# Kernel optimization log

Hardware: AMD Instinct MI355X
Metric: run time of the kernel (lower is better)

Reference implementation:

```python
import jax, jax.numpy as jnp
import numpy as np

R = 0.15          # ball-query radius (module init arg r)
K = 32            # _MAX_NEIGHBOURS
B, N = 8, 4096


def _ball_query(pos, r, k):
    """Dense ball query. pos: [B,N,3] -> neighbor idx [B,N,K], sorted by distance.
    Slots with fewer than k in-radius neighbors are filled with the query's own
    index (self is always the first neighbor at distance 0), so their
    contribution to (f_i - f_j)^2 is exactly 0 -- matching torch-points-kernels'
    fill-with-first-neighbor behaviour."""
    d2 = jnp.sum((pos[:, :, None, :] - pos[:, None, :, :]) ** 2, axis=-1)  # [B,N,N]
    masked = jnp.where(d2 <= r * r, d2, jnp.inf)
    neg_vals, idx = jax.lax.top_k(-masked, k)          # ascending distance
    valid = neg_vals > -jnp.inf
    self_idx = jnp.arange(pos.shape[1])[None, :, None]
    return jnp.where(valid, idx, self_idx)             # [B,N,K]


def setup_inputs() -> dict:
    key = jax.random.key(0)
    k1, k2 = jax.random.split(key)
    pos = jax.random.uniform(k1, (B, N, 3), dtype=jnp.float32)
    f = jax.random.normal(k2, (B, N), dtype=jnp.float32)
    return {"pos": pos, "f": f}


def reference(pos, f):
    # neighbor indices are non-differentiable (torch gathers with long indices)
    nei_idx = jax.lax.stop_gradient(_ball_query(pos, R, K))      # [B,N,K]
    f_nei = jax.vmap(lambda fb, ib: fb[ib])(f, nei_idx)          # [B,N,K]
    variances = jnp.sum((f[:, :, None] - f_nei) ** 2, axis=-1)   # [B,N]
    return 0.5 * jnp.mean(variances)
```

## Files before the change

### kernel.cpp

```cpp
#include <hip/hip_runtime.h>


#define BQ_K 32
#define CAP 128
#define WPB 8
#define G 6
#define NC (G * G * G)
#define CAPC 512
#define QMAX 64
#define NPTS 4096
#define NPART 64
#define PSTRIDE 16

__device__ __forceinline__ int cell_coord(float x) {
    int c = (int)(x * (float)G);
    return c < 0 ? 0 : (c > G - 1 ? G - 1 : c);
}

__device__ __forceinline__ unsigned int decode_cnt(unsigned int v) {
    return (v >= 0x80000000u) ? (v - 0xAAAAAAAAu) : v;
}

__device__ __forceinline__ float select_sum(float2 e0, float2 e1, int M,
                                            float r2) {
    if (M <= BQ_K) return e0.y + e1.y;
    float lo = 0.0f, hi = r2 * 1.000001f;
    #pragma unroll
    for (int it = 0; it < 12; ++it) {
        const float mid = 0.5f * (lo + hi);
        const int cnt = __popcll(__ballot(e0.x < mid)) +
                        __popcll(__ballot(e1.x < mid));
        if (cnt >= BQ_K) hi = mid; else lo = mid;
    }
    float s = 0.0f;
    if (e0.x < hi) s = e0.y;
    if (e1.x < hi) s += e1.y;
    return s;
}

__device__ __forceinline__ float dual_select_sum(
    float2 a0, float2 a1, int MA, float2 b0, float2 b1, int MB, float r2)
{
    const bool needA = MA > BQ_K;
    const bool needB = MB > BQ_K;
    float hiA = 1e31f, hiB = 1e31f;
    if (needA || needB) {
        float loA = 0.0f, loB = 0.0f;
        if (needA) hiA = r2 * 1.000001f;
        if (needB) hiB = r2 * 1.000001f;
        const bool bigA = MA > 64, bigB = MB > 64;
        #pragma unroll
        for (int it = 0; it < 12; ++it) {
            if (needA) {
                const float mid = 0.5f * (loA + hiA);
                int c = __popcll(__ballot(a0.x < mid));
                if (bigA) c += __popcll(__ballot(a1.x < mid));
                if (c >= BQ_K) hiA = mid; else loA = mid;
            }
            if (needB) {
                const float mid = 0.5f * (loB + hiB);
                int c = __popcll(__ballot(b0.x < mid));
                if (bigB) c += __popcll(__ballot(b1.x < mid));
                if (c >= BQ_K) hiB = mid; else loB = mid;
            }
        }
    }
    float s = 0.0f;
    if (a0.x < hiA) s += a0.y;
    if (a1.x < hiA) s += a1.y;
    if (b0.x < hiB) s += b0.y;
    if (b1.x < hiB) s += b1.y;
    return s;
}

__global__ __launch_bounds__(512, 8) void dl_fused8(
    const float* __restrict__ pos, const float* __restrict__ f,
    float* __restrict__ partial, unsigned int* __restrict__ c1,
    unsigned int* __restrict__ c2, float* __restrict__ out,
    float r2, float scale)
{
    __shared__ float4 s_cand[CAPC];
    __shared__ float2 s_sel[WPB][2][CAP];
    __shared__ int    s_q[QMAX];
    __shared__ int    s_ncand, s_nq;
    __shared__ float  s_wsum[WPB];
    __shared__ int    s_last;

    const int bc = blockIdx.x;
    const int b  = bc / NC;
    const int c  = bc - b * NC;
    const int cx = c % G, cy = (c / G) % G, cz = c / (G * G);

    const int lane = threadIdx.x & 63;
    const int wave = threadIdx.x >> 6;
    const unsigned long long lmask = (1ULL << lane) - 1ULL;

    if (threadIdx.x == 0) { s_ncand = 0; s_nq = 0; s_last = 0; }
    __syncthreads();

    const float* posb = pos + (size_t)b * NPTS * 3;
    const float* fb   = f   + (size_t)b * NPTS;

    const float lox = cx * (1.0f / G), hix = lox + (1.0f / G);
    const float loy = cy * (1.0f / G), hiy = loy + (1.0f / G);
    const float loz = cz * (1.0f / G), hiz = loz + (1.0f / G);

    constexpr int per = NPTS / WPB;
    const int wbeg = wave * per;
    for (int j0 = 0; j0 < per; j0 += 128) {
        const int ja = wbeg + j0 + lane;
        const int jb = ja + 64;
        const float xa = posb[3 * ja + 0];
        const float ya = posb[3 * ja + 1];
        const float za = posb[3 * ja + 2];
        const float fa = fb[ja];
        const float xb = posb[3 * jb + 0];
        const float yb = posb[3 * jb + 1];
        const float zb = posb[3 * jb + 2];
        const float fvb = fb[jb];

        const float dax = fmaxf(fmaxf(lox - xa, xa - hix), 0.0f);
        const float day = fmaxf(fmaxf(loy - ya, ya - hiy), 0.0f);
        const float daz = fmaxf(fmaxf(loz - za, za - hiz), 0.0f);
        const float d2a = fmaf(dax, dax, fmaf(day, day, daz * daz));
        const float dbx = fmaxf(fmaxf(lox - xb, xb - hix), 0.0f);
        const float dby = fmaxf(fmaxf(loy - yb, yb - hiy), 0.0f);
        const float dbz = fmaxf(fmaxf(loz - zb, zb - hiz), 0.0f);
        const float d2b = fmaf(dbx, dbx, fmaf(dby, dby, dbz * dbz));
        const bool ina = d2a <= r2;
        const bool inb = d2b <= r2;

        const unsigned long long ma = __ballot(ina);
        const unsigned long long mb = __ballot(inb);
        const int na = __popcll(ma);
        const int nh = na + __popcll(mb);
        int base = 0;
        if (lane == 0 && nh) base = atomicAdd(&s_ncand, nh);
        base = __shfl(base, 0, 64);
        if (ina) {
            const int off = base + __popcll(ma & lmask);
            if (off < CAPC) {
                s_cand[off] = make_float4(xa, ya, za, fa);
                if (cell_coord(xa) == cx && cell_coord(ya) == cy &&
                    cell_coord(za) == cz) {
                    const int qs = atomicAdd(&s_nq, 1);
                    if (qs < QMAX) s_q[qs] = off;
                }
            }
        }
        if (inb) {
            const int off = base + na + __popcll(mb & lmask);
            if (off < CAPC) {
                s_cand[off] = make_float4(xb, yb, zb, fvb);
                if (cell_coord(xb) == cx && cell_coord(yb) == cy &&
                    cell_coord(zb) == cz) {
                    const int qs = atomicAdd(&s_nq, 1);
                    if (qs < QMAX) s_q[qs] = off;
                }
            }
        }
    }
    __syncthreads();

    const int ncand = s_ncand < CAPC ? s_ncand : CAPC;
    const int nq    = s_nq < QMAX ? s_nq : QMAX;
    const int ncB   = (ncand + 63) & ~63;

    for (int i = ncand + threadIdx.x; i < ncB; i += 512)
        s_cand[i] = make_float4(1e30f, 1e30f, 1e30f, 0.0f);
    __syncthreads();

    float2* selA = s_sel[wave][0];
    float2* selB = s_sel[wave][1];
    float wsum = 0.0f;

    for (int qi = 2 * wave; qi < nq; qi += 2 * WPB) {
        const int  qj    = qi + 1;
        const bool haveB = qj < nq;
        const float4 qpA = s_cand[s_q[qi]];
        const float4 qpB = s_cand[s_q[haveB ? qj : qi]];
        const float qxA = qpA.x, qyA = qpA.y, qzA = qpA.z, fiA = qpA.w;
        const float qxB = qpB.x, qyB = qpB.y, qzB = qpB.z, fiB = qpB.w;

        int cinA = 0, cinB = 0;
        for (int basej = 0; basej < ncB; basej += 64) {
            const float4 cd = s_cand[basej + lane];
            const float dxA = cd.x - qxA, dyA = cd.y - qyA, dzA = cd.z - qzA;
            const float dxB = cd.x - qxB, dyB = cd.y - qyB, dzB = cd.z - qzB;
            const float d2A = fmaf(dxA, dxA, fmaf(dyA, dyA, dzA * dzA));
            const float d2B = fmaf(dxB, dxB, fmaf(dyB, dyB, dzB * dzB));
            const bool inbA = d2A <= r2;
            const bool inbB = haveB && (d2B <= r2);
            const unsigned long long mA = __ballot(inbA);
            const unsigned long long mB = __ballot(inbB);
            const int offA = cinA + __popcll(mA & lmask);
            const int offB = cinB + __popcll(mB & lmask);
            if (inbA && offA < CAP) {
                const float fd = fiA - cd.w;
                selA[offA] = make_float2(d2A, fd * fd);
            }
            if (inbB && offB < CAP) {
                const float fd = fiB - cd.w;
                selB[offB] = make_float2(d2B, fd * fd);
            }
            cinA += __popcll(mA);
            cinB += __popcll(mB);
        }
        const int MA = cinA < CAP ? cinA : CAP;
        const int MB = cinB < CAP ? cinB : CAP;
        const float2 a0 = (lane < MA) ? selA[lane] : make_float2(1e30f, 0.0f);
        const float2 a1 = (64 + lane < MA) ? selA[64 + lane]
                                           : make_float2(1e30f, 0.0f);
        const float2 b0 = (lane < MB) ? selB[lane] : make_float2(1e30f, 0.0f);
        const float2 b1 = (64 + lane < MB) ? selB[64 + lane]
                                           : make_float2(1e30f, 0.0f);
        wsum += dual_select_sum(a0, a1, MA, b0, b1, MB, r2);
    }

    for (int o = 32; o > 0; o >>= 1) wsum += __shfl_down(wsum, o, 64);
    if (lane == 0) s_wsum[wave] = wsum;
    __syncthreads();
    if (threadIdx.x == 0) {
        float bs = 0.0f;
        #pragma unroll
        for (int w = 0; w < WPB; ++w) bs += s_wsum[w];
        const int k = blockIdx.x & (NPART - 1);
        const float oldp = atomicAdd(&partial[k * PSTRIDE], bs);
        asm volatile("" :: "v"(oldp));
        const unsigned int expect = (gridDim.x - 1u - (unsigned)k) / 64u + 1u;
        const unsigned int oc =
            decode_cnt(atomicAdd(&c1[k * PSTRIDE], 1u));
        if (oc + 1u == expect) {
            const unsigned int o2 = decode_cnt(atomicAdd(c2, 1u));
            if (o2 + 1u == (unsigned)NPART)
                s_last = 1;
        }
    }
    __syncthreads();
    if (s_last && wave == 0) {
        float v = atomicAdd(&partial[lane * PSTRIDE], 0.0f);
        for (int o = 32; o > 0; o >>= 1) v += __shfl_down(v, o, 64);
        if (lane == 0) out[0] = v * scale;
    }
}

__global__ __launch_bounds__(256) void dl_fallback(
    const float* __restrict__ pos, const float* __restrict__ f,
    float* __restrict__ out, float r2, float scale)
{
    __shared__ float4 s_cand[CAPC];
    __shared__ float2 s_sel[4][CAP];
    __shared__ int    s_q[QMAX];
    __shared__ int    s_ncand, s_nq;
    __shared__ float  s_wsum[4];

    const int bc = blockIdx.x;
    const int b  = bc / NC;
    const int c  = bc - b * NC;
    const int cx = c % G, cy = (c / G) % G, cz = c / (G * G);
    const int lane = threadIdx.x & 63;
    const int wave = threadIdx.x >> 6;
    const unsigned long long lmask = (1ULL << lane) - 1ULL;

    if (threadIdx.x == 0) { s_ncand = 0; s_nq = 0; }
    __syncthreads();

    const float* posb = pos + (size_t)b * NPTS * 3;
    const float* fb   = f   + (size_t)b * NPTS;
    const float lox = cx * (1.0f / G), hix = lox + (1.0f / G);
    const float loy = cy * (1.0f / G), hiy = loy + (1.0f / G);
    const float loz = cz * (1.0f / G), hiz = loz + (1.0f / G);

    constexpr int per = NPTS / 4;
    const int wbeg = wave * per;
    for (int j0 = 0; j0 < per; j0 += 64) {
        const int j = wbeg + j0 + lane;
        const float x  = posb[3 * j + 0];
        const float y  = posb[3 * j + 1];
        const float z  = posb[3 * j + 2];
        const float ddx = fmaxf(fmaxf(lox - x, x - hix), 0.0f);
        const float ddy = fmaxf(fmaxf(loy - y, y - hiy), 0.0f);
        const float ddz = fmaxf(fmaxf(loz - z, z - hiz), 0.0f);
        const float d2c = fmaf(ddx, ddx, fmaf(ddy, ddy, ddz * ddz));
        const bool in = (d2c <= r2);
        const unsigned long long m = __ballot(in);
        const int nh = __popcll(m);
        int base = 0;
        if (lane == 0 && nh) base = atomicAdd(&s_ncand, nh);
        base = __shfl(base, 0, 64);
        if (in) {
            const int off = base + __popcll(m & lmask);
            if (off < CAPC) {
                s_cand[off] = make_float4(x, y, z, fb[j]);
                if (cell_coord(x) == cx && cell_coord(y) == cy &&
                    cell_coord(z) == cz) {
                    const int qs = atomicAdd(&s_nq, 1);
                    if (qs < QMAX) s_q[qs] = off;
                }
            }
        }
    }
    __syncthreads();

    const int ncand = s_ncand < CAPC ? s_ncand : CAPC;
    const int nq    = s_nq < QMAX ? s_nq : QMAX;
    const int ncB   = (ncand + 63) & ~63;
    float2* sel = s_sel[wave];
    float wsum = 0.0f;

    for (int qi = wave; qi < nq; qi += 4) {
        const float4 qp = s_cand[s_q[qi]];
        const float qx = qp.x, qy = qp.y, qz = qp.z, fi = qp.w;
        int cin = 0;
        for (int basej = 0; basej < ncB; basej += 64) {
            const float4 cd = s_cand[basej + lane];
            const bool valid = (basej + lane) < ncand;
            const float dx = cd.x - qx, dy = cd.y - qy, dz = cd.z - qz;
            const float d2 = fmaf(dx, dx, fmaf(dy, dy, dz * dz));
            const bool inb = valid && (d2 <= r2);
            const unsigned long long mm = __ballot(inb);
            const int off = cin + __popcll(mm & lmask);
            if (inb && off < CAP) {
                const float fd = fi - cd.w;
                sel[off] = make_float2(d2, fd * fd);
            }
            cin += __popcll(mm);
        }
        const int M = cin < CAP ? cin : CAP;
        const float2 e0 = (lane < M) ? sel[lane] : make_float2(1e30f, 0.0f);
        const float2 e1 = (64 + lane < M) ? sel[64 + lane]
                                          : make_float2(1e30f, 0.0f);
        wsum += select_sum(e0, e1, M, r2);
    }

    for (int o = 32; o > 0; o >>= 1) wsum += __shfl_down(wsum, o, 64);
    if (lane == 0) s_wsum[wave] = wsum;
    __syncthreads();
    if (threadIdx.x == 0) {
        const float bs = s_wsum[0] + s_wsum[1] + s_wsum[2] + s_wsum[3];
        atomicAdd(out, bs * scale);
    }
}

extern "C" void kernel_launch(void* const* d_in, const int* in_sizes, int n_in,
                              void* d_out, int out_size, void* d_ws, size_t ws_size,
                              hipStream_t stream) {
    const float* pos = (const float*)d_in[0];
    const float* f   = (const float*)d_in[1];
    float* out = (float*)d_out;

    const int B = in_sizes[1] / NPTS;
    const int total = B * NPTS;
    const float r2 = 0.15f * 0.15f;
    const float scale = 0.5f / (float)total;

    const size_t part_bytes = (size_t)NPART * PSTRIDE * sizeof(float);
    const size_t c1_bytes   = (size_t)NPART * PSTRIDE * sizeof(unsigned);
    const size_t c2_bytes   = 64;
    if (ws_size < part_bytes + c1_bytes + c2_bytes) {
        hipMemsetAsync(out, 0, sizeof(float), stream);
        dl_fallback<<<B * NC, 256, 0, stream>>>(pos, f, out, r2, scale);
        return;
    }

    char* wsp = (char*)d_ws;
    float*        partial = (float*)wsp;
    unsigned int* c1      = (unsigned int*)(wsp + part_bytes);
    unsigned int* c2      = (unsigned int*)(wsp + part_bytes + c1_bytes);

    dl_fused8<<<B * NC, 512, 0, stream>>>(pos, f, partial, c1, c2, out,
                                          r2, scale);
}
```

Before: 77.41 us.

## Convert per-cell grid into persistent blocks pulling cells from per-batch atomic queue

New measurement: 80.14 us. 1.04x slower.

```diff
diff --git a/kernel.cpp b/kernel.cpp
--- a/kernel.cpp
+++ b/kernel.cpp
@@ -11,6 +11,7 @@
 #define NPTS 4096
 #define NPART 64
 #define PSTRIDE 16
+#define BLKS_PER_BATCH 128
 
 __device__ __forceinline__ int cell_coord(float x) {
     int c = (int)(x * (float)G);
@@ -73,11 +74,11 @@
     return s;
 }
 
-__global__ __launch_bounds__(512, 8) void dl_fused8(
+__global__ __launch_bounds__(512, 8) void dl_persist(
     const float* __restrict__ pos, const float* __restrict__ f,
     float* __restrict__ partial, unsigned int* __restrict__ c1,
-    unsigned int* __restrict__ c2, float* __restrict__ out,
-    float r2, float scale)
+    unsigned int* __restrict__ c2, unsigned int* __restrict__ qctr,
+    float* __restrict__ out, float r2, float scale, int ncells)
 {
     __shared__ float4 s_cand[CAPC];
     __shared__ float2 s_sel[WPB][2][CAP];
@@ -85,162 +86,175 @@
     __shared__ int    s_ncand, s_nq;
     __shared__ float  s_wsum[WPB];
     __shared__ int    s_last;
-
-    const int bc = blockIdx.x;
-    const int b  = bc / NC;
-    const int c  = bc - b * NC;
-    const int cx = c % G, cy = (c / G) % G, cz = c / (G * G);
-
+    __shared__ int    s_ci;
+
+    const int batch = blockIdx.x >> 7;
     const int lane = threadIdx.x & 63;
     const int wave = threadIdx.x >> 6;
     const unsigned long long lmask = (1ULL << lane) - 1ULL;
 
-    if (threadIdx.x == 0) { s_ncand = 0; s_nq = 0; s_last = 0; }
-    __syncthreads();
-
-    const float* posb = pos + (size_t)b * NPTS * 3;
-    const float* fb   = f   + (size_t)b * NPTS;
-
-    const float lox = cx * (1.0f / G), hix = lox + (1.0f / G);
-    const float loy = cy * (1.0f / G), hiy = loy + (1.0f / G);
-    const float loz = cz * (1.0f / G), hiz = loz + (1.0f / G);
-
-    constexpr int per = NPTS / WPB;
-    const int wbeg = wave * per;
-    for (int j0 = 0; j0 < per; j0 += 128) {
-        const int ja = wbeg + j0 + lane;
-        const int jb = ja + 64;
-        const float xa = posb[3 * ja + 0];
-        const float ya = posb[3 * ja + 1];
-        const float za = posb[3 * ja + 2];
-        const float fa = fb[ja];
-        const float xb = posb[3 * jb + 0];
-        const float yb = posb[3 * jb + 1];
-        const float zb = posb[3 * jb + 2];
-        const float fvb = fb[jb];
-
-        const float dax = fmaxf(fmaxf(lox - xa, xa - hix), 0.0f);
-        const float day = fmaxf(fmaxf(loy - ya, ya - hiy), 0.0f);
-        const float daz = fmaxf(fmaxf(loz - za, za - hiz), 0.0f);
-        const float d2a = fmaf(dax, dax, fmaf(day, day, daz * daz));
-        const float dbx = fmaxf(fmaxf(lox - xb, xb - hix), 0.0f);
-        const float dby = fmaxf(fmaxf(loy - yb, yb - hiy), 0.0f);
-        const float dbz = fmaxf(fmaxf(loz - zb, zb - hiz), 0.0f);
-        const float d2b = fmaf(dbx, dbx, fmaf(dby, dby, dbz * dbz));
-        const bool ina = d2a <= r2;
-        const bool inb = d2b <= r2;
-
-        const unsigned long long ma = __ballot(ina);
-        const unsigned long long mb = __ballot(inb);
-        const int na = __popcll(ma);
-        const int nh = na + __popcll(mb);
-        int base = 0;
-        if (lane == 0 && nh) base = atomicAdd(&s_ncand, nh);
-        base = __shfl(base, 0, 64);
-        if (ina) {
-            const int off = base + __popcll(ma & lmask);
-            if (off < CAPC) {
-                s_cand[off] = make_float4(xa, ya, za, fa);
-                if (cell_coord(xa) == cx && cell_coord(ya) == cy &&
-                    cell_coord(za) == cz) {
-                    const int qs = atomicAdd(&s_nq, 1);
-                    if (qs < QMAX) s_q[qs] = off;
-                }
-            }
-        }
-        if (inb) {
-            const int off = base + na + __popcll(mb & lmask);
-            if (off < CAPC) {
-                s_cand[off] = make_float4(xb, yb, zb, fvb);
-                if (cell_coord(xb) == cx && cell_coord(yb) == cy &&
-                    cell_coord(zb) == cz) {
-                    const int qs = atomicAdd(&s_nq, 1);
-                    if (qs < QMAX) s_q[qs] = off;
-                }
-            }
-        }
-    }
-    __syncthreads();
-
-    const int ncand = s_ncand < CAPC ? s_ncand : CAPC;
-    const int nq    = s_nq < QMAX ? s_nq : QMAX;
-    const int ncB   = (ncand + 63) & ~63;
-
-    for (int i = ncand + threadIdx.x; i < ncB; i += 512)
-        s_cand[i] = make_float4(1e30f, 1e30f, 1e30f, 0.0f);
-    __syncthreads();
-
-    float2* selA = s_sel[wave][0];
-    float2* selB = s_sel[wave][1];
-    float wsum = 0.0f;
-
-    for (int qi = 2 * wave; qi < nq; qi += 2 * WPB) {
-        const int  qj    = qi + 1;
-        const bool haveB = qj < nq;
-        const float4 qpA = s_cand[s_q[qi]];
-        const float4 qpB = s_cand[s_q[haveB ? qj : qi]];
-        const float qxA = qpA.x, qyA = qpA.y, qzA = qpA.z, fiA = qpA.w;
-        const float qxB = qpB.x, qyB = qpB.y, qzB = qpB.z, fiB = qpB.w;
-
-        int cinA = 0, cinB = 0;
-        for (int basej = 0; basej < ncB; basej += 64) {
-            const float4 cd = s_cand[basej + lane];
-            const float dxA = cd.x - qxA, dyA = cd.y - qyA, dzA = cd.z - qzA;
-            const float dxB = cd.x - qxB, dyB = cd.y - qyB, dzB = cd.z - qzB;
-            const float d2A = fmaf(dxA, dxA, fmaf(dyA, dyA, dzA * dzA));
-            const float d2B = fmaf(dxB, dxB, fmaf(dyB, dyB, dzB * dzB));
-            const bool inbA = d2A <= r2;
-            const bool inbB = haveB && (d2B <= r2);
-            const unsigned long long mA = __ballot(inbA);
-            const unsigned long long mB = __ballot(inbB);
-            const int offA = cinA + __popcll(mA & lmask);
-            const int offB = cinB + __popcll(mB & lmask);
-            if (inbA && offA < CAP) {
-                const float fd = fiA - cd.w;
-                selA[offA] = make_float2(d2A, fd * fd);
-            }
-            if (inbB && offB < CAP) {
-                const float fd = fiB - cd.w;
-                selB[offB] = make_float2(d2B, fd * fd);
-            }
-            cinA += __popcll(mA);
-            cinB += __popcll(mB);
-        }
-        const int MA = cinA < CAP ? cinA : CAP;
-        const int MB = cinB < CAP ? cinB : CAP;
-        const float2 a0 = (lane < MA) ? selA[lane] : make_float2(1e30f, 0.0f);
-        const float2 a1 = (64 + lane < MA) ? selA[64 + lane]
-                                           : make_float2(1e30f, 0.0f);
-        const float2 b0 = (lane < MB) ? selB[lane] : make_float2(1e30f, 0.0f);
-        const float2 b1 = (64 + lane < MB) ? selB[64 + lane]
-                                           : make_float2(1e30f, 0.0f);
-        wsum += dual_select_sum(a0, a1, MA, b0, b1, MB, r2);
-    }
-
-    for (int o = 32; o > 0; o >>= 1) wsum += __shfl_down(wsum, o, 64);
-    if (lane == 0) s_wsum[wave] = wsum;
-    __syncthreads();
-    if (threadIdx.x == 0) {
-        float bs = 0.0f;
-        #pragma unroll
-        for (int w = 0; w < WPB; ++w) bs += s_wsum[w];
-        const int k = blockIdx.x & (NPART - 1);
-        const float oldp = atomicAdd(&partial[k * PSTRIDE], bs);
-        asm volatile("" :: "v"(oldp));
-        const unsigned int expect = (gridDim.x - 1u - (unsigned)k) / 64u + 1u;
-        const unsigned int oc =
-            decode_cnt(atomicAdd(&c1[k * PSTRIDE], 1u));
-        if (oc + 1u == expect) {
-            const unsigned int o2 = decode_cnt(atomicAdd(c2, 1u));
-            if (o2 + 1u == (unsigned)NPART)
-                s_last = 1;
-        }
-    }
-    __syncthreads();
-    if (s_last && wave == 0) {
-        float v = atomicAdd(&partial[lane * PSTRIDE], 0.0f);
-        for (int o = 32; o > 0; o >>= 1) v += __shfl_down(v, o, 64);
-        if (lane == 0) out[0] = v * scale;
+    const float* posb = pos + (size_t)batch * NPTS * 3;
+    const float* fb   = f   + (size_t)batch * NPTS;
+
+    for (;;) {
+        __syncthreads();
+        if (threadIdx.x == 0) {
+            const unsigned int raw = atomicAdd(&qctr[batch * PSTRIDE], 1u);
+            s_ci = (int)decode_cnt(raw);
+            s_ncand = 0; s_nq = 0; s_last = 0;
+        }
+        __syncthreads();
+        const int ci = s_ci;
+        if (ci >= NC) break;
+
+        const int cx = ci % G, cy = (ci / G) % G, cz = ci / (G * G);
+        const float lox = cx * (1.0f / G), hix = lox + (1.0f / G);
+        const float loy = cy * (1.0f / G), hiy = loy + (1.0f / G);
+        const float loz = cz * (1.0f / G), hiz = loz + (1.0f / G);
+
+        constexpr int per = NPTS / WPB;
+        const int wbeg = wave * per;
+        for (int j0 = 0; j0 < per; j0 += 128) {
+            const int ja = wbeg + j0 + lane;
+            const int jb = ja + 64;
+            const float xa = posb[3 * ja + 0];
+            const float ya = posb[3 * ja + 1];
+            const float za = posb[3 * ja + 2];
+            const float fa = fb[ja];
+            const float xb = posb[3 * jb + 0];
+            const float yb = posb[3 * jb + 1];
+            const float zb = posb[3 * jb + 2];
+            const float fvb = fb[jb];
+
+            const float dax = fmaxf(fmaxf(lox - xa, xa - hix), 0.0f);
+            const float day = fmaxf(fmaxf(loy - ya, ya - hiy), 0.0f);
+            const float daz = fmaxf(fmaxf(loz - za, za - hiz), 0.0f);
+            const float d2a = fmaf(dax, dax, fmaf(day, day, daz * daz));
+            const float dbx = fmaxf(fmaxf(lox - xb, xb - hix), 0.0f);
+            const float dby = fmaxf(fmaxf(loy - yb, yb - hiy), 0.0f);
+            const float dbz = fmaxf(fmaxf(loz - zb, zb - hiz), 0.0f);
+            const float d2b = fmaf(dbx, dbx, fmaf(dby, dby, dbz * dbz));
+            const bool ina = d2a <= r2;
+            const bool inb = d2b <= r2;
+
+            const unsigned long long ma = __ballot(ina);
+            const unsigned long long mb = __ballot(inb);
+            const int na = __popcll(ma);
+            const int nh = na + __popcll(mb);
+            int base = 0;
+            if (lane == 0 && nh) base = atomicAdd(&s_ncand, nh);
+            base = __shfl(base, 0, 64);
+            if (ina) {
+                const int off = base + __popcll(ma & lmask);
+                if (off < CAPC) {
+                    s_cand[off] = make_float4(xa, ya, za, fa);
+                    if (cell_coord(xa) == cx && cell_coord(ya) == cy &&
+                        cell_coord(za) == cz) {
+                        const int qs = atomicAdd(&s_nq, 1);
+                        if (qs < QMAX) s_q[qs] = off;
+                    }
+                }
+            }
+            if (inb) {
+                const int off = base + na + __popcll(mb & lmask);
+                if (off < CAPC) {
+                    s_cand[off] = make_float4(xb, yb, zb, fvb);
+                    if (cell_coord(xb) == cx && cell_coord(yb) == cy &&
+                        cell_coord(zb) == cz) {
+                        const int qs = atomicAdd(&s_nq, 1);
+                        if (qs < QMAX) s_q[qs] = off;
+                    }
+                }
+            }
+        }
+        __syncthreads();
+
+        const int ncand = s_ncand < CAPC ? s_ncand : CAPC;
+        const int nq    = s_nq < QMAX ? s_nq : QMAX;
+        const int ncB   = (ncand + 63) & ~63;
+
+        for (int i = ncand + threadIdx.x; i < ncB; i += 512)
+            s_cand[i] = make_float4(1e30f, 1e30f, 1e30f, 0.0f);
+        __syncthreads();
+
+        float2* selA = s_sel[wave][0];
+        float2* selB = s_sel[wave][1];
+        float wsum = 0.0f;
+
+        for (int qi = 2 * wave; qi < nq; qi += 2 * WPB) {
+            const int  qj    = qi + 1;
+            const bool haveB = qj < nq;
+            const float4 qpA = s_cand[s_q[qi]];
+            const float4 qpB = s_cand[s_q[haveB ? qj : qi]];
+            const float qxA = qpA.x, qyA = qpA.y, qzA = qpA.z, fiA = qpA.w;
+            const float qxB = qpB.x, qyB = qpB.y, qzB = qpB.z, fiB = qpB.w;
+
+            int cinA = 0, cinB = 0;
+            for (int basej = 0; basej < ncB; basej += 64) {
+                const float4 cd = s_cand[basej + lane];
+                const float dxA = cd.x - qxA, dyA = cd.y - qyA,
+                            dzA = cd.z - qzA;
+                const float dxB = cd.x - qxB, dyB = cd.y - qyB,
+                            dzB = cd.z - qzB;
+                const float d2A = fmaf(dxA, dxA, fmaf(dyA, dyA, dzA * dzA));
+                const float d2B = fmaf(dxB, dxB, fmaf(dyB, dyB, dzB * dzB));
+                const bool inbA = d2A <= r2;
+                const bool inbB = haveB && (d2B <= r2);
+                const unsigned long long mA = __ballot(inbA);
+                const unsigned long long mB = __ballot(inbB);
+                const int offA = cinA + __popcll(mA & lmask);
+                const int offB = cinB + __popcll(mB & lmask);
+                if (inbA && offA < CAP) {
+                    const float fd = fiA - cd.w;
+                    selA[offA] = make_float2(d2A, fd * fd);
+                }
+                if (inbB && offB < CAP) {
+                    const float fd = fiB - cd.w;
+                    selB[offB] = make_float2(d2B, fd * fd);
+                }
+                cinA += __popcll(mA);
+                cinB += __popcll(mB);
+            }
+            const int MA = cinA < CAP ? cinA : CAP;
+            const int MB = cinB < CAP ? cinB : CAP;
+            const float2 a0 = (lane < MA) ? selA[lane]
+                                          : make_float2(1e30f, 0.0f);
+            const float2 a1 = (64 + lane < MA) ? selA[64 + lane]
+                                               : make_float2(1e30f, 0.0f);
+            const float2 b0 = (lane < MB) ? selB[lane]
+                                          : make_float2(1e30f, 0.0f);
+            const float2 b1 = (64 + lane < MB) ? selB[64 + lane]
+                                               : make_float2(1e30f, 0.0f);
+            wsum += dual_select_sum(a0, a1, MA, b0, b1, MB, r2);
+        }
+
+        for (int o = 32; o > 0; o >>= 1) wsum += __shfl_down(wsum, o, 64);
+        if (lane == 0) s_wsum[wave] = wsum;
+        __syncthreads();
+        if (threadIdx.x == 0) {
+            float bs = 0.0f;
+            #pragma unroll
+            for (int w = 0; w < WPB; ++w) bs += s_wsum[w];
+            const int g = batch * NC + ci;
+            const int k = g & (NPART - 1);
+            const float oldp = atomicAdd(&partial[k * PSTRIDE], bs);
+            asm volatile("" :: "v"(oldp));
+            const unsigned int expect =
+                ((unsigned)ncells - 1u - (unsigned)k) / 64u + 1u;
+            const unsigned int oc =
+                decode_cnt(atomicAdd(&c1[k * PSTRIDE], 1u));
+            if (oc + 1u == expect) {
+                const unsigned int o2 = decode_cnt(atomicAdd(c2, 1u));
+                if (o2 + 1u == (unsigned)NPART)
+                    s_last = 1;
+            }
+        }
+        __syncthreads();
+        if (s_last && wave == 0) {
+            float v = atomicAdd(&partial[lane * PSTRIDE], 0.0f);
+            for (int o = 32; o > 0; o >>= 1) v += __shfl_down(v, o, 64);
+            if (lane == 0) out[0] = v * scale;
+        }
     }
 }
 
@@ -357,7 +371,8 @@
     const size_t part_bytes = (size_t)NPART * PSTRIDE * sizeof(float);
     const size_t c1_bytes   = (size_t)NPART * PSTRIDE * sizeof(unsigned);
     const size_t c2_bytes   = 64;
-    if (ws_size < part_bytes + c1_bytes + c2_bytes) {
+    const size_t q_bytes    = (size_t)B * PSTRIDE * sizeof(unsigned);
+    if (ws_size < part_bytes + c1_bytes + c2_bytes + q_bytes) {
         hipMemsetAsync(out, 0, sizeof(float), stream);
         dl_fallback<<<B * NC, 256, 0, stream>>>(pos, f, out, r2, scale);
         return;
@@ -367,7 +382,9 @@
     float*        partial = (float*)wsp;
     unsigned int* c1      = (unsigned int*)(wsp + part_bytes);
     unsigned int* c2      = (unsigned int*)(wsp + part_bytes + c1_bytes);
-
-    dl_fused8<<<B * NC, 512, 0, stream>>>(pos, f, partial, c1, c2, out,
-                                          r2, scale);
-}
+    unsigned int* qctr    = (unsigned int*)(wsp + part_bytes + c1_bytes +
+                                            c2_bytes);
+
+    dl_persist<<<B * BLKS_PER_BATCH, 512, 0, stream>>>(
+        pos, f, partial, c1, c2, qctr, out, r2, scale, B * NC);
+}
```
